# Performance work log

Hardware: AMD Instinct MI355X
Metric: run time of the kernel (lower is better)

The kernel has to match this reference:

```python
import jax, jax.numpy as jnp
import numpy as np

B, N, D = 8, 2048, 1024
H, HD, FF = 16, 32, 4096  # head_dim = D // H // 2 = 32
LAMBDA_INIT = float(0.8 - 0.6 * np.exp(-0.3 * 1.0))  # layer_num = 1
EPS = 1e-5


def setup_inputs() -> dict:
    key = jax.random.key(0)
    ks = jax.random.split(key, 24)
    g = lambda k, shape, std=0.02: (jax.random.normal(k, shape, jnp.float32) * std)
    return {
        "src": jax.random.normal(ks[0], (B, N, D), jnp.float32),
        "Wq": g(ks[1], (D, D)), "Wk": g(ks[2], (D, D)), "Wv": g(ks[3], (D, D)),
        "Wo": g(ks[4], (D, D)), "bo": jnp.zeros((D,), jnp.float32),
        "lq1": g(ks[5], (HD,), 0.1), "lq2": g(ks[6], (HD,), 0.1),
        "lk1": g(ks[7], (HD,), 0.1), "lk2": g(ks[8], (HD,), 0.1),
        "ln1_g": jnp.ones((D,), jnp.float32), "ln1_b": jnp.zeros((D,), jnp.float32),
        "ln2_g": jnp.ones((D,), jnp.float32), "ln2_b": jnp.zeros((D,), jnp.float32),
        "W1": g(ks[9], (FF, D)), "b1": jnp.zeros((FF,), jnp.float32),
        "W2": g(ks[10], (D, FF)), "b2": jnp.zeros((D,), jnp.float32),
        "Wr": g(ks[11], (D, D)), "Ur": g(ks[12], (D, D)),
        "Wz": g(ks[13], (D, D)), "Uz": g(ks[14], (D, D)),
        "Wg": g(ks[15], (D, D)), "Ug": g(ks[16], (D, D)),
        "bg": jnp.full((D,), 2.0, jnp.float32),
    }


def _layernorm(x, gamma, beta):
    m = x.mean(-1, keepdims=True)
    v = jnp.mean((x - m) ** 2, axis=-1, keepdims=True)
    return (x - m) * jax.lax.rsqrt(v + EPS) * gamma + beta


def _diff_attn(x, Wq, Wk, Wv, Wo, bo, lq1, lq2, lk1, lk2):
    b, n, d = x.shape
    scale = HD ** -0.5
    # 'b n (h d q) -> b n (q h) d'
    q = (x @ Wq.T).reshape(b, n, H, HD, 2).transpose(0, 1, 4, 2, 3).reshape(b, n, 2 * H, HD) * scale
    # 'b n (h d k) -> b n (k h) d'
    k = (x @ Wk.T).reshape(b, n, H, HD, 2).transpose(0, 1, 4, 2, 3).reshape(b, n, 2 * H, HD)
    # 'b n (h d) -> b h n d', d = 2*HD
    v = (x @ Wv.T).reshape(b, n, H, 2 * HD).transpose(0, 2, 1, 3)
    # per-token attention over the 2H head axis: [b, n, 2H, 2H]
    att = jnp.einsum('bnqd,bnkd->bnqk', q, k)
    att = jax.nn.softmax(att.astype(jnp.float32), axis=-1)
    lam = jnp.exp(jnp.sum(lq1 * lk1)) - jnp.exp(jnp.sum(lq2 * lk2)) + LAMBDA_INIT
    att = att.reshape(b, n, 2, H, 2, H)  # q k split
    diff = att[:, :, 0, :, 0, :] - lam * att[:, :, 1, :, 1, :]  # [b, n, H, H]
    out = jnp.einsum('bnah,bhnd->bnad', diff, v)  # [b, n, H, 2*HD]
    # RMSNorm over last dim, no affine
    out = out * jax.lax.rsqrt(jnp.mean(out ** 2, axis=-1, keepdims=True) + EPS)
    out = (out * (1.0 - LAMBDA_INIT)).reshape(b, n, d)
    return out @ Wo.T + bo


def _gate_gru(x, y, Wr, Ur, Wz, Uz, Wg, Ug, bg):
    r = jax.nn.sigmoid(y @ Wr.T + x @ Ur.T)
    z = jax.nn.sigmoid(y @ Wz.T + x @ Uz.T - bg)
    h = jnp.tanh(y @ Wg.T + (r * x) @ Ug.T)
    return (1.0 - z) * x + z * h


def reference(src, Wq, Wk, Wv, Wo, bo, lq1, lq2, lk1, lk2,
              ln1_g, ln1_b, ln2_g, ln2_b, W1, b1, W2, b2,
              Wr, Ur, Wz, Uz, Wg, Ug, bg):
    # norm_first=True, use_gate=True (GRU), wo_ffn=False, dropout=0 (eval)
    s = _layernorm(src, ln1_g, ln1_b)
    src2 = _diff_attn(s, Wq, Wk, Wv, Wo, bo, lq1, lq2, lk1, lk2)
    conn = _gate_gru(src, jax.nn.relu(src2), Wr, Ur, Wz, Uz, Wg, Ug, bg)
    c = _layernorm(conn, ln2_g, ln2_b)
    src3 = jax.nn.relu(c @ W1.T + b1) @ W2.T + b2
    conn2 = _gate_gru(conn, jax.nn.relu(src3), Wr, Ur, Wz, Uz, Wg, Ug, bg)
    return conn2
```

## Files before the change

kernel.cpp:

```cpp
#include <hip/hip_runtime.h>


#define DEV __device__ __forceinline__

typedef unsigned short u16;
typedef __bf16 bf16x8 __attribute__((ext_vector_type(8)));
typedef float f32x4 __attribute__((ext_vector_type(4)));
typedef unsigned short us8 __attribute__((ext_vector_type(8)));
typedef unsigned short us4 __attribute__((ext_vector_type(4)));

#define LAMBDA0            0.35550906759096928f
#define ONE_MINUS_LAMBDA0  0.6444909324090307f
#define QSCALE             0.17677669529663687f

DEV float bf2f(u16 u) { union { unsigned u; float f; } x; x.u = ((unsigned)u) << 16; return x.f; }
DEV u16 f2bf(float f) {
  union { float f; unsigned u; } x; x.f = f;
  unsigned r = x.u + 0x7FFFu + ((x.u >> 16) & 1u);
  return (u16)(r >> 16);
}

DEV void gl_lds16(const void* g, void* l) {
  __builtin_amdgcn_global_load_lds((__attribute__((address_space(1))) void*)g,
                                   (__attribute__((address_space(3))) void*)l, 16, 0, 0);
}

#define MF(a, b, c) __builtin_amdgcn_mfma_f32_16x16x32_bf16(a, b, c, 0, 0, 0)
#define BARM() asm volatile("s_barrier" ::: "memory")

DEV void stage_half_f(const u16* __restrict__ g, int ld, int rowbase, int k0,
                      u16* lds, int bufoff , int h, int wave, int lane)
{
  const int rr = lane >> 3;
  const int sc = ((lane & 7) ^ rr) * 8;
  const u16* gs = g + (size_t)(rowbase + h * 128 + wave * 16 + rr) * ld + (k0 + sc);
  u16* l = lds + bufoff + h * 8192 + wave * 1024;
  gl_lds16(gs, l);
  gl_lds16(gs + (size_t)8 * ld, l + 512);
}

template <int ACT, int OBF>
__global__ __launch_bounds__(512, 2)
void gemm256(const u16* __restrict__ A, int lda, const u16* __restrict__ W,
             const float* __restrict__ bias, void* __restrict__ outp,
             int ldo, int K)
{
  __shared__ u16 As[32768];
  __shared__ u16 Bs[32768];

  const int tid = threadIdx.x;
  const int lane = tid & 63, wave = tid >> 6;
  const int wr = wave >> 2, wc = wave & 3;
  const int frow = lane & 15, fx = lane >> 4, s7 = lane & 7;

  const int gx = gridDim.x;
  const int nwg = gx * gridDim.y;
  const int lin = blockIdx.y * gx + blockIdx.x;
  const int logical = (lin & 7) * (nwg >> 3) + (lin >> 3);
  const int m0 = (logical / gx) * 256;
  const int n0 = (logical % gx) * 256;

  const int NT = K >> 6;
  const int aoff = (wr * 32 + frow) * 64;
  const int boff = (wc * 64 + frow) * 64;
  const int swA0 = (fx ^ s7) * 8;
  const int swA1 = ((4 + fx) ^ s7) * 8;

  f32x4 acc[8][4] = {};
  bf16x8 bfr[4][2];

  stage_half_f(W, K, n0, 0, Bs, 0, 0, wave, lane);
  stage_half_f(W, K, n0, 0, Bs, 0, 1, wave, lane);
  stage_half_f(A, lda, m0, 0, As, 0, 0, wave, lane);
  stage_half_f(A, lda, m0, 0, As, 0, 1, wave, lane);
  stage_half_f(W, K, n0, 64, Bs, 16384, 0, wave, lane);
  stage_half_f(W, K, n0, 64, Bs, 16384, 1, wave, lane);
  asm volatile("s_waitcnt vmcnt(6)" ::: "memory");
  BARM();

#define PH(q, STG, TAILW)                                                     \
  {                                                                           \
    bf16x8 a00 = *(const bf16x8*)(As + aB + 4096 * (q) + swA0);               \
    bf16x8 a01 = *(const bf16x8*)(As + aB + 4096 * (q) + swA1);               \
    bf16x8 a10 = *(const bf16x8*)(As + aB + 4096 * (q) + 1024 + swA0);        \
    bf16x8 a11 = *(const bf16x8*)(As + aB + 4096 * (q) + 1024 + swA1);        \
    STG;                                                                      \
    BARM();                                                                   \
    __builtin_amdgcn_s_setprio(1);                                            \
    acc[2*(q)  ][0] = MF(a00, bfr[0][0], acc[2*(q)  ][0]);                    \
    acc[2*(q)  ][1] = MF(a00, bfr[1][0], acc[2*(q)  ][1]);                    \
    acc[2*(q)  ][2] = MF(a00, bfr[2][0], acc[2*(q)  ][2]);                    \
    acc[2*(q)  ][3] = MF(a00, bfr[3][0], acc[2*(q)  ][3]);                    \
    acc[2*(q)+1][0] = MF(a10, bfr[0][0], acc[2*(q)+1][0]);                    \
    acc[2*(q)+1][1] = MF(a10, bfr[1][0], acc[2*(q)+1][1]);                    \
    acc[2*(q)+1][2] = MF(a10, bfr[2][0], acc[2*(q)+1][2]);                    \
    acc[2*(q)+1][3] = MF(a10, bfr[3][0], acc[2*(q)+1][3]);                    \
    acc[2*(q)  ][0] = MF(a01, bfr[0][1], acc[2*(q)  ][0]);                    \
    acc[2*(q)  ][1] = MF(a01, bfr[1][1], acc[2*(q)  ][1]);                    \
    acc[2*(q)  ][2] = MF(a01, bfr[2][1], acc[2*(q)  ][2]);                    \
    acc[2*(q)  ][3] = MF(a01, bfr[3][1], acc[2*(q)  ][3]);                    \
    acc[2*(q)+1][0] = MF(a11, bfr[0][1], acc[2*(q)+1][0]);                    \
    acc[2*(q)+1][1] = MF(a11, bfr[1][1], acc[2*(q)+1][1]);                    \
    acc[2*(q)+1][2] = MF(a11, bfr[2][1], acc[2*(q)+1][2]);                    \
    acc[2*(q)+1][3] = MF(a11, bfr[3][1], acc[2*(q)+1][3]);                    \
    __builtin_amdgcn_s_setprio(0);                                            \
    TAILW;                                                                    \
    BARM();                                                                   \
  }

  for (int t = 0; t < NT; ++t) {
    const int cb = (t & 1) * 16384;
    const int ob = 16384 - cb;
    const int kA = ((t + 1 < NT) ? t + 1 : NT - 1) * 64;
    const int kB = ((t + 2 < NT) ? t + 2 : NT - 1) * 64;
    const int aB = cb + aoff;
    const int bB = cb + boff;
#pragma unroll
    for (int n = 0; n < 4; ++n) {
      bfr[n][0] = *(const bf16x8*)(Bs + bB + n * 1024 + swA0);
      bfr[n][1] = *(const bf16x8*)(Bs + bB + n * 1024 + swA1);
    }
    PH(0, stage_half_f(A, lda, m0, kA, As, ob, 0, wave, lane), (void)0);
    PH(1, stage_half_f(A, lda, m0, kA, As, ob, 1, wave, lane),
       asm volatile("s_waitcnt vmcnt(8)" ::: "memory"));
    PH(2, stage_half_f(W, K, n0, kB, Bs, cb, 0, wave, lane), (void)0);
    PH(3, stage_half_f(W, K, n0, kB, Bs, cb, 1, wave, lane),
       asm volatile("s_waitcnt vmcnt(6)" ::: "memory"));
  }
#undef PH

  const int er = fx * 4;
#pragma unroll
  for (int q = 0; q < 4; ++q)
#pragma unroll
    for (int j = 0; j < 2; ++j) {
      const int grb = m0 + 64 * q + wr * 32 + j * 16 + er;
#pragma unroll
      for (int n = 0; n < 4; ++n) {
        const int gc = n0 + wc * 64 + n * 16 + frow;
        const float bv = bias ? bias[gc] : 0.f;
#pragma unroll
        for (int tt = 0; tt < 4; ++tt) {
          float v = acc[2 * q + j][n][tt] + bv;
          if (ACT == 1) v = fmaxf(v, 0.f);
          else if (ACT == 2) v = 1.f / (1.f + expf(-v));
          else if (ACT == 3) v = tanhf(v);
          if (OBF) ((u16*)outp)[(size_t)(grb + tt) * ldo + gc] = f2bf(v);
          else     ((float*)outp)[(size_t)(grb + tt) * ldo + gc] = v;
        }
      }
    }
}

__global__ __launch_bounds__(256)
void ln_kernel(const float* __restrict__ in, const float* __restrict__ g,
               const float* __restrict__ b, u16* __restrict__ out)
{
  const int row = blockIdx.x, tid = threadIdx.x;
  const float4 x = ((const float4*)(in + (size_t)row * 1024))[tid];
  float s = x.x + x.y + x.z + x.w;
  float sq = x.x * x.x + x.y * x.y + x.z * x.z + x.w * x.w;
#pragma unroll
  for (int o = 32; o >= 1; o >>= 1) { s += __shfl_xor(s, o); sq += __shfl_xor(sq, o); }
  __shared__ float ls[4], lq[4];
  const int wave = tid >> 6;
  if ((tid & 63) == 0) { ls[wave] = s; lq[wave] = sq; }
  __syncthreads();
  s = ls[0] + ls[1] + ls[2] + ls[3];
  sq = lq[0] + lq[1] + lq[2] + lq[3];
  const float mean = s * (1.f / 1024.f);
  const float rstd = rsqrtf(sq * (1.f / 1024.f) - mean * mean + 1e-5f);
  const float4 gg = ((const float4*)g)[tid];
  const float4 bb = ((const float4*)b)[tid];
  us4 ov;
  ov[0] = f2bf((x.x - mean) * rstd * gg.x + bb.x);
  ov[1] = f2bf((x.y - mean) * rstd * gg.y + bb.y);
  ov[2] = f2bf((x.z - mean) * rstd * gg.z + bb.z);
  ov[3] = f2bf((x.w - mean) * rstd * gg.w + bb.w);
  *(us4*)(out + (size_t)row * 1024 + tid * 4) = ov;
}

__global__ __launch_bounds__(256)
void combine_ln_kernel(const float* __restrict__ x, const float* __restrict__ rzh,
                       const float* __restrict__ g, const float* __restrict__ b,
                       float* __restrict__ conn, u16* __restrict__ catbase)
{
  const int row = blockIdx.x, tid = threadIdx.x;
  const float4 xv = ((const float4*)(x + (size_t)row * 1024))[tid];
  const float4 hv = *(const float4*)(rzh + (size_t)row * 2048 + tid * 4);
  const float4 zv = *(const float4*)(rzh + (size_t)row * 2048 + 1024 + tid * 4);
  float4 cv;
  cv.x = (1.f - zv.x) * xv.x + zv.x * hv.x;
  cv.y = (1.f - zv.y) * xv.y + zv.y * hv.y;
  cv.z = (1.f - zv.z) * xv.z + zv.z * hv.z;
  cv.w = (1.f - zv.w) * xv.w + zv.w * hv.w;
  ((float4*)(conn + (size_t)row * 1024))[tid] = cv;
  us4 cb; cb[0] = f2bf(cv.x); cb[1] = f2bf(cv.y); cb[2] = f2bf(cv.z); cb[3] = f2bf(cv.w);
  *(us4*)(catbase + (size_t)row * 2048 + 1024 + tid * 4) = cb;

  float s = cv.x + cv.y + cv.z + cv.w;
  float sq = cv.x * cv.x + cv.y * cv.y + cv.z * cv.z + cv.w * cv.w;
#pragma unroll
  for (int o = 32; o >= 1; o >>= 1) { s += __shfl_xor(s, o); sq += __shfl_xor(sq, o); }
  __shared__ float ls[4], lq[4];
  const int wave = tid >> 6;
  if ((tid & 63) == 0) { ls[wave] = s; lq[wave] = sq; }
  __syncthreads();
  s = ls[0] + ls[1] + ls[2] + ls[3];
  sq = lq[0] + lq[1] + lq[2] + lq[3];
  const float mean = s * (1.f / 1024.f);
  const float rstd = rsqrtf(sq * (1.f / 1024.f) - mean * mean + 1e-5f);
  const float4 gg = ((const float4*)g)[tid];
  const float4 bb = ((const float4*)b)[tid];
  us4 ov;
  ov[0] = f2bf((cv.x - mean) * rstd * gg.x + bb.x);
  ov[1] = f2bf((cv.y - mean) * rstd * gg.y + bb.y);
  ov[2] = f2bf((cv.z - mean) * rstd * gg.z + bb.z);
  ov[3] = f2bf((cv.w - mean) * rstd * gg.w + bb.w);
  *(us4*)(catbase + (size_t)row * 2048 + tid * 4) = ov;
}

__global__ __launch_bounds__(256)
void combine2_kernel(const float* __restrict__ x, const float* __restrict__ rzh,
                     float* __restrict__ out)
{
  const int t = blockIdx.x * 256 + threadIdx.x;
  const int row = t >> 8;
  const int c4 = (t & 255) * 4;
  const float4 hv = *(const float4*)(rzh + (size_t)row * 2048 + c4);
  const float4 zv = *(const float4*)(rzh + (size_t)row * 2048 + 1024 + c4);
  const float4 xv = *(const float4*)(x + (size_t)row * 1024 + c4);
  float4 o;
  o.x = (1.f - zv.x) * xv.x + zv.x * hv.x;
  o.y = (1.f - zv.y) * xv.y + zv.y * hv.y;
  o.z = (1.f - zv.z) * xv.z + zv.z * hv.z;
  o.w = (1.f - zv.w) * xv.w + zv.w * hv.w;
  *(float4*)(out + (size_t)row * 1024 + c4) = o;
}

__global__ __launch_bounds__(256)
void rx_kernel(const float* __restrict__ rzh, const float* __restrict__ x,
               u16* __restrict__ dst)
{
  const int t = blockIdx.x * 256 + threadIdx.x;
  const int row = t >> 8;
  const int c4 = (t & 255) * 4;
  const float4 rv = *(const float4*)(rzh + (size_t)row * 2048 + c4);
  const float4 xv = *(const float4*)(x + (size_t)row * 1024 + c4);
  us4 o;
  o[0] = f2bf(rv.x * xv.x); o[1] = f2bf(rv.y * xv.y);
  o[2] = f2bf(rv.z * xv.z); o[3] = f2bf(rv.w * xv.w);
  *(us4*)(dst + (size_t)row * 2048 + c4) = o;
}

__global__ __launch_bounds__(256)
void cvt2d_kernel(const float* __restrict__ src, u16* __restrict__ dst,
                  int total4, int cshift, int ldd)
{
  const int t = blockIdx.x * 256 + threadIdx.x;
  if (t >= total4) return;
  const int idx = t * 4;
  const int r = idx >> cshift;
  const int c = idx & ((1 << cshift) - 1);
  const float4 v = *(const float4*)(src + (size_t)idx);
  us4 o; o[0] = f2bf(v.x); o[1] = f2bf(v.y); o[2] = f2bf(v.z); o[3] = f2bf(v.w);
  *(us4*)(dst + (size_t)r * ldd + c) = o;
}

__global__ __launch_bounds__(256)
void biasrz_kernel(const float* __restrict__ bg, float* __restrict__ brz)
{
  const int t = blockIdx.x * 256 + threadIdx.x;
  brz[t] = (t < 1024) ? 0.f : -bg[t - 1024];
}

__global__ __launch_bounds__(256)
void sentinel_kernel(float* __restrict__ out, int n)
{
  const int t = blockIdx.x * 256 + threadIdx.x;
  if (t < n) out[t] = 1.0e9f;
}

__global__ __launch_bounds__(256)
void attn_kernel(const u16* __restrict__ qkv,
                 const float* __restrict__ lq1, const float* __restrict__ lq2,
                 const float* __restrict__ lk1, const float* __restrict__ lk2,
                 u16* __restrict__ out)
{
  __shared__ float k_s[4][32][36];
  __shared__ float att_s[4][32][33];
  const int wave = threadIdx.x >> 6, lane = threadIdx.x & 63;
  const int tok = blockIdx.x * 4 + wave;
  const u16* qrow = qkv + (size_t)tok * 3072;
  const u16* krow = qrow + 1024;
  const u16* vrow = qrow + 2048;

  {
    us8 a = *(const us8*)(krow + lane * 16);
    us8 b = *(const us8*)(krow + lane * 16 + 8);
#pragma unroll
    for (int j = 0; j < 16; ++j) {
      int e = lane * 16 + j;
      u16 usv = (j < 8) ? a[j] : b[j - 8];
      int h = e >> 6, r = e & 63;
      k_s[wave][(r & 1) * 16 + h][r >> 1] = bf2f(usv);
    }
  }
  float qr[32];
  {
    const int a = lane & 31, h = a & 15, qi = a >> 4;
#pragma unroll
    for (int s = 0; s < 8; ++s) {
      us8 v8 = *(const us8*)(qrow + h * 64 + s * 8);
#pragma unroll
      for (int u = 0; u < 4; ++u) qr[s * 4 + u] = bf2f(v8[2 * u + qi]) * QSCALE;
    }
  }
  float lam;
  {
    const int dd = lane & 31;
    float p1 = lq1[dd] * lk1[dd], p2 = lq2[dd] * lk2[dd];
#pragma unroll
    for (int o = 16; o >= 1; o >>= 1) { p1 += __shfl_xor(p1, o); p2 += __shfl_xor(p2, o); }
    lam = expf(p1) - expf(p2) + LAMBDA0;
  }
  __syncthreads();

  const int a = lane & 31, bb = (lane >> 5) * 16;
  float av[16];
#pragma unroll
  for (int bi = 0; bi < 16; ++bi) {
    const float4* kk = (const float4*)&k_s[wave][bb + bi][0];
    float s = 0.f;
#pragma unroll
    for (int d4 = 0; d4 < 8; ++d4) {
      float4 kv = kk[d4];
      s += qr[d4 * 4 + 0] * kv.x + qr[d4 * 4 + 1] * kv.y +
           qr[d4 * 4 + 2] * kv.z + qr[d4 * 4 + 3] * kv.w;
    }
    av[bi] = s;
  }
  float mx = av[0];
#pragma unroll
  for (int i = 1; i < 16; ++i) mx = fmaxf(mx, av[i]);
  mx = fmaxf(mx, __shfl_xor(mx, 32));
  float se = 0.f;
#pragma unroll
  for (int i = 0; i < 16; ++i) { av[i] = expf(av[i] - mx); se += av[i]; }
  se += __shfl_xor(se, 32);
  const float inv = 1.f / se;
#pragma unroll
  for (int i = 0; i < 16; ++i) att_s[wave][a][bb + i] = av[i] * inv;
  __syncthreads();

  const int a2 = lane >> 2, jb = (lane & 3) * 16;
  float o[16];
#pragma unroll
  for (int j = 0; j < 16; ++j) o[j] = 0.f;
#pragma unroll
  for (int h = 0; h < 16; ++h) {
    const float dc = att_s[wave][a2][h] - lam * att_s[wave][16 + a2][16 + h];
    const u16* vv = vrow + h * 64 + jb;
    us8 v0 = *(const us8*)vv;
    us8 v1 = *(const us8*)(vv + 8);
#pragma unroll
    for (int j = 0; j < 8; ++j) { o[j] += dc * bf2f(v0[j]); o[8 + j] += dc * bf2f(v1[j]); }
  }
  float ss = 0.f;
#pragma unroll
  for (int j = 0; j < 16; ++j) ss += o[j] * o[j];
  ss += __shfl_xor(ss, 1);
  ss += __shfl_xor(ss, 2);
  const float sc = rsqrtf(ss * (1.f / 64.f) + 1e-5f) * ONE_MINUS_LAMBDA0;
  us8 r0, r1;
#pragma unroll
  for (int j = 0; j < 8; ++j) { r0[j] = f2bf(o[j] * sc); r1[j] = f2bf(o[8 + j] * sc); }
  u16* op = out + (size_t)tok * 1024 + a2 * 64 + jb;
  *(us8*)op = r0;
  *(us8*)(op + 8) = r1;
}

enum : size_t {
  OFF_WQKV = 0,
  OFF_WO   = OFF_WQKV + (size_t)3072 * 1024 * 2,
  OFF_WRZ  = OFF_WO   + (size_t)1024 * 1024 * 2,
  OFF_WG   = OFF_WRZ  + (size_t)2048 * 2048 * 2,
  OFF_W1   = OFF_WG   + (size_t)1024 * 2048 * 2,
  OFF_W2   = OFF_W1   + (size_t)4096 * 1024 * 2,
  OFF_BRZ  = OFF_W2   + (size_t)1024 * 4096 * 2,
  OFF_R1   = OFF_BRZ  + (size_t)2048 * 4,
  OFF_CAT  = OFF_R1   + (size_t)134217728,
  WS_NEED  = OFF_CAT  + (size_t)16384 * 2048 * 2
};

extern "C" void kernel_launch(void* const* d_in, const int* in_sizes, int n_in,
                              void* d_out, int out_size, void* d_ws, size_t ws_size,
                              hipStream_t stream)
{
  (void)in_sizes; (void)n_in;
  if (ws_size < WS_NEED) {
    sentinel_kernel<<<(out_size + 255) / 256, 256, 0, stream>>>((float*)d_out, out_size);
    return;
  }

  const float* src  = (const float*)d_in[0];
  const float* Wq   = (const float*)d_in[1];
  const float* Wk   = (const float*)d_in[2];
  const float* Wv   = (const float*)d_in[3];
  const float* Wo   = (const float*)d_in[4];
  const float* bo   = (const float*)d_in[5];
  const float* lq1  = (const float*)d_in[6];
  const float* lq2  = (const float*)d_in[7];
  const float* lk1  = (const float*)d_in[8];
  const float* lk2  = (const float*)d_in[9];
  const float* ln1g = (const float*)d_in[10];
  const float* ln1b = (const float*)d_in[11];
  const float* ln2g = (const float*)d_in[12];
  const float* ln2b = (const float*)d_in[13];
  const float* W1   = (const float*)d_in[14];
  const float* b1   = (const float*)d_in[15];
  const float* W2   = (const float*)d_in[16];
  const float* b2   = (const float*)d_in[17];
  const float* Wr   = (const float*)d_in[18];
  const float* Ur   = (const float*)d_in[19];
  const float* Wz   = (const float*)d_in[20];
  const float* Uz   = (const float*)d_in[21];
  const float* Wg   = (const float*)d_in[22];
  const float* Ug   = (const float*)d_in[23];
  const float* bg   = (const float*)d_in[24];

  char* ws = (char*)d_ws;
  u16*   wqkv = (u16*)(ws + OFF_WQKV);
  u16*   wo_b = (u16*)(ws + OFF_WO);
  u16*   wrz  = (u16*)(ws + OFF_WRZ);
  u16*   wgc  = (u16*)(ws + OFF_WG);
  u16*   w1b  = (u16*)(ws + OFF_W1);
  u16*   w2b  = (u16*)(ws + OFF_W2);
  float* brz  = (float*)(ws + OFF_BRZ);
  u16*   r1u  = (u16*)(ws + OFF_R1);
  u16*   sbuf = (u16*)(ws + OFF_R1 + 100663296);
  float* rzh  = (float*)(ws + OFF_R1);
  u16*   cat  = (u16*)(ws + OFF_CAT);
  float* conn = (float*)d_out;

  auto cvt = [&](const float* s, u16* dst, int rows, int cshift, int ldd) {
    int total4 = (rows << cshift) >> 2;
    cvt2d_kernel<<<(total4 + 255) / 256, 256, 0, stream>>>(s, dst, total4, cshift, ldd);
  };

  cvt(Wq, wqkv,                     1024, 10, 1024);
  cvt(Wk, wqkv + 1024 * 1024,       1024, 10, 1024);
  cvt(Wv, wqkv + 2 * 1024 * 1024,   1024, 10, 1024);
  cvt(Wo, wo_b,                     1024, 10, 1024);
  cvt(Wr, wrz,                      1024, 10, 2048);
  cvt(Ur, wrz + 1024,               1024, 10, 2048);
  cvt(Wz, wrz + 2048 * 1024,        1024, 10, 2048);
  cvt(Uz, wrz + 2048 * 1024 + 1024, 1024, 10, 2048);
  cvt(Wg, wgc,                      1024, 10, 2048);
  cvt(Ug, wgc + 1024,               1024, 10, 2048);
  cvt(W1, w1b,                      4096, 10, 1024);
  cvt(W2, w2b,                      1024, 12, 4096);
  cvt(src, cat + 1024,             16384, 10, 2048);
  biasrz_kernel<<<8, 256, 0, stream>>>(bg, brz);

  ln_kernel<<<16384, 256, 0, stream>>>(src, ln1g, ln1b, sbuf);

  gemm256<0, 1><<<dim3(12, 64), 512, 0, stream>>>(sbuf, 1024, wqkv, nullptr, r1u, 3072, 1024);

  attn_kernel<<<4096, 256, 0, stream>>>(r1u, lq1, lq2, lk1, lk2, sbuf);

  gemm256<1, 1><<<dim3(4, 64), 512, 0, stream>>>(sbuf, 1024, wo_b, bo, cat, 2048, 1024);

  gemm256<2, 0><<<dim3(8, 64), 512, 0, stream>>>(cat, 2048, wrz, brz, rzh, 2048, 2048);
  rx_kernel<<<16384, 256, 0, stream>>>(rzh, src, cat + 1024);
  gemm256<3, 0><<<dim3(4, 64), 512, 0, stream>>>(cat, 2048, wgc, nullptr, rzh, 2048, 2048);
  combine_ln_kernel<<<16384, 256, 0, stream>>>(src, rzh, ln2g, ln2b, conn, cat);

  gemm256<1, 1><<<dim3(16, 64), 512, 0, stream>>>(cat, 2048, w1b, b1, r1u, 4096, 1024);
  gemm256<1, 1><<<dim3(4, 64), 512, 0, stream>>>(r1u, 4096, w2b, b2, cat, 2048, 4096);

  gemm256<2, 0><<<dim3(8, 64), 512, 0, stream>>>(cat, 2048, wrz, brz, rzh, 2048, 2048);
  rx_kernel<<<16384, 256, 0, stream>>>(rzh, conn, cat + 1024);
  gemm256<3, 0><<<dim3(4, 64), 512, 0, stream>>>(cat, 2048, wgc, nullptr, rzh, 2048, 2048);
  combine2_kernel<<<16384, 256, 0, stream>>>(conn, rzh, (float*)d_out);
}
```

Before: 1.318 ms.

## Switch GEMM to 32x32x16 MFMA tiles with reworked LDS pipeline

Replaces the 16x16x32 bf16 MFMA inner loop with 32x32x16 MFMA, reorganising per-wave fragments into 4x2 32x32 accumulators and loading B fragments once per K tile. The staging schedule is restructured into two phases per K step, with A prefetch issued up front and W prefetch in the second phase and adjusted vmcnt waits. The epilogue is rewritten for the 32x32 output layout. Larger MFMA tiles reduce LDS fragment reads per FLOP, at the risk of a changed pipeline overlap and more register pressure.

```diff
diff --git a/kernel.cpp b/kernel.cpp
--- a/kernel.cpp
+++ b/kernel.cpp
@@ -6,6 +6,7 @@
 typedef unsigned short u16;
 typedef __bf16 bf16x8 __attribute__((ext_vector_type(8)));
 typedef float f32x4 __attribute__((ext_vector_type(4)));
+typedef float f32x16 __attribute__((ext_vector_type(16)));
 typedef unsigned short us8 __attribute__((ext_vector_type(8)));
 typedef unsigned short us4 __attribute__((ext_vector_type(4)));
 
@@ -25,7 +26,7 @@
                                    (__attribute__((address_space(3))) void*)l, 16, 0, 0);
 }
 
-#define MF(a, b, c) __builtin_amdgcn_mfma_f32_16x16x32_bf16(a, b, c, 0, 0, 0)
+#define MF32(a, b, c) __builtin_amdgcn_mfma_f32_32x32x16_bf16(a, b, c, 0, 0, 0)
 #define BARM() asm volatile("s_barrier" ::: "memory")
 
 DEV void stage_half_f(const u16* __restrict__ g, int ld, int rowbase, int k0,
@@ -51,7 +52,7 @@
   const int tid = threadIdx.x;
   const int lane = tid & 63, wave = tid >> 6;
   const int wr = wave >> 2, wc = wave & 3;
-  const int frow = lane & 15, fx = lane >> 4, s7 = lane & 7;
+  const int r31 = lane & 31, fx32 = lane >> 5, l7 = lane & 7;
 
   const int gx = gridDim.x;
   const int nwg = gx * gridDim.y;
@@ -61,48 +62,53 @@
   const int n0 = (logical % gx) * 256;
 
   const int NT = K >> 6;
-  const int aoff = (wr * 32 + frow) * 64;
-  const int boff = (wc * 64 + frow) * 64;
-  const int swA0 = (fx ^ s7) * 8;
-  const int swA1 = ((4 + fx) ^ s7) * 8;
-
-  f32x4 acc[8][4] = {};
-  bf16x8 bfr[4][2];
-
+  const int sw[4] = { ((0 + fx32) ^ l7) * 8, ((2 + fx32) ^ l7) * 8,
+                      ((4 + fx32) ^ l7) * 8, ((6 + fx32) ^ l7) * 8 };
+  const int arow = (wr * 32 + r31) * 64;
+  const int brow = (wc * 64 + r31) * 64;
+
+  f32x16 acc[4][2] = {};
+  bf16x8 bb[2][4];
+
+  stage_half_f(A, lda, m0, 0, As, 0, 0, wave, lane);
+  stage_half_f(A, lda, m0, 0, As, 0, 1, wave, lane);
   stage_half_f(W, K, n0, 0, Bs, 0, 0, wave, lane);
   stage_half_f(W, K, n0, 0, Bs, 0, 1, wave, lane);
-  stage_half_f(A, lda, m0, 0, As, 0, 0, wave, lane);
-  stage_half_f(A, lda, m0, 0, As, 0, 1, wave, lane);
   stage_half_f(W, K, n0, 64, Bs, 16384, 0, wave, lane);
   stage_half_f(W, K, n0, 64, Bs, 16384, 1, wave, lane);
-  asm volatile("s_waitcnt vmcnt(6)" ::: "memory");
+  asm volatile("s_waitcnt vmcnt(4)" ::: "memory");
   BARM();
 
-#define PH(q, STG, TAILW)                                                     \
+#define PH32(p, STG, TAILW)                                                   \
   {                                                                           \
-    bf16x8 a00 = *(const bf16x8*)(As + aB + 4096 * (q) + swA0);               \
-    bf16x8 a01 = *(const bf16x8*)(As + aB + 4096 * (q) + swA1);               \
-    bf16x8 a10 = *(const bf16x8*)(As + aB + 4096 * (q) + 1024 + swA0);        \
-    bf16x8 a11 = *(const bf16x8*)(As + aB + 4096 * (q) + 1024 + swA1);        \
     STG;                                                                      \
+    const int mb = cb + (p) * 8192 + arow;                                    \
+    bf16x8 a00 = *(const bf16x8*)(As + mb + sw[0]);                           \
+    bf16x8 a01 = *(const bf16x8*)(As + mb + sw[1]);                           \
+    bf16x8 a02 = *(const bf16x8*)(As + mb + sw[2]);                           \
+    bf16x8 a03 = *(const bf16x8*)(As + mb + sw[3]);                           \
+    bf16x8 a10 = *(const bf16x8*)(As + mb + 4096 + sw[0]);                    \
+    bf16x8 a11 = *(const bf16x8*)(As + mb + 4096 + sw[1]);                    \
+    bf16x8 a12 = *(const bf16x8*)(As + mb + 4096 + sw[2]);                    \
+    bf16x8 a13 = *(const bf16x8*)(As + mb + 4096 + sw[3]);                    \
     BARM();                                                                   \
     __builtin_amdgcn_s_setprio(1);                                            \
-    acc[2*(q)  ][0] = MF(a00, bfr[0][0], acc[2*(q)  ][0]);                    \
-    acc[2*(q)  ][1] = MF(a00, bfr[1][0], acc[2*(q)  ][1]);                    \
-    acc[2*(q)  ][2] = MF(a00, bfr[2][0], acc[2*(q)  ][2]);                    \
-    acc[2*(q)  ][3] = MF(a00, bfr[3][0], acc[2*(q)  ][3]);                    \
-    acc[2*(q)+1][0] = MF(a10, bfr[0][0], acc[2*(q)+1][0]);                    \
-    acc[2*(q)+1][1] = MF(a10, bfr[1][0], acc[2*(q)+1][1]);                    \
-    acc[2*(q)+1][2] = MF(a10, bfr[2][0], acc[2*(q)+1][2]);                    \
-    acc[2*(q)+1][3] = MF(a10, bfr[3][0], acc[2*(q)+1][3]);                    \
-    acc[2*(q)  ][0] = MF(a01, bfr[0][1], acc[2*(q)  ][0]);                    \
-    acc[2*(q)  ][1] = MF(a01, bfr[1][1], acc[2*(q)  ][1]);                    \
-    acc[2*(q)  ][2] = MF(a01, bfr[2][1], acc[2*(q)  ][2]);                    \
-    acc[2*(q)  ][3] = MF(a01, bfr[3][1], acc[2*(q)  ][3]);                    \
-    acc[2*(q)+1][0] = MF(a11, bfr[0][1], acc[2*(q)+1][0]);                    \
-    acc[2*(q)+1][1] = MF(a11, bfr[1][1], acc[2*(q)+1][1]);                    \
-    acc[2*(q)+1][2] = MF(a11, bfr[2][1], acc[2*(q)+1][2]);                    \
-    acc[2*(q)+1][3] = MF(a11, bfr[3][1], acc[2*(q)+1][3]);                    \
+    acc[2*(p)  ][0] = MF32(a00, bb[0][0], acc[2*(p)  ][0]);                   \
+    acc[2*(p)  ][1] = MF32(a00, bb[1][0], acc[2*(p)  ][1]);                   \
+    acc[2*(p)+1][0] = MF32(a10, bb[0][0], acc[2*(p)+1][0]);                   \
+    acc[2*(p)+1][1] = MF32(a10, bb[1][0], acc[2*(p)+1][1]);                   \
+    acc[2*(p)  ][0] = MF32(a01, bb[0][1], acc[2*(p)  ][0]);                   \
+    acc[2*(p)  ][1] = MF32(a01, bb[1][1], acc[2*(p)  ][1]);                   \
+    acc[2*(p)+1][0] = MF32(a11, bb[0][1], acc[2*(p)+1][0]);                   \
+    acc[2*(p)+1][1] = MF32(a11, bb[1][1], acc[2*(p)+1][1]);                   \
+    acc[2*(p)  ][0] = MF32(a02, bb[0][2], acc[2*(p)  ][0]);                   \
+    acc[2*(p)  ][1] = MF32(a02, bb[1][2], acc[2*(p)  ][1]);                   \
+    acc[2*(p)+1][0] = MF32(a12, bb[0][2], acc[2*(p)+1][0]);                   \
+    acc[2*(p)+1][1] = MF32(a12, bb[1][2], acc[2*(p)+1][1]);                   \
+    acc[2*(p)  ][0] = MF32(a03, bb[0][3], acc[2*(p)  ][0]);                   \
+    acc[2*(p)  ][1] = MF32(a03, bb[1][3], acc[2*(p)  ][1]);                   \
+    acc[2*(p)+1][0] = MF32(a13, bb[0][3], acc[2*(p)+1][0]);                   \
+    acc[2*(p)+1][1] = MF32(a13, bb[1][3], acc[2*(p)+1][1]);                   \
     __builtin_amdgcn_s_setprio(0);                                            \
     TAILW;                                                                    \
     BARM();                                                                   \
@@ -113,41 +119,38 @@
     const int ob = 16384 - cb;
     const int kA = ((t + 1 < NT) ? t + 1 : NT - 1) * 64;
     const int kB = ((t + 2 < NT) ? t + 2 : NT - 1) * 64;
-    const int aB = cb + aoff;
-    const int bB = cb + boff;
-#pragma unroll
-    for (int n = 0; n < 4; ++n) {
-      bfr[n][0] = *(const bf16x8*)(Bs + bB + n * 1024 + swA0);
-      bfr[n][1] = *(const bf16x8*)(Bs + bB + n * 1024 + swA1);
+    {
+      stage_half_f(A, lda, m0, kA, As, ob, 0, wave, lane);
+      stage_half_f(A, lda, m0, kA, As, ob, 1, wave, lane);
+#pragma unroll
+      for (int nj = 0; nj < 2; ++nj)
+#pragma unroll
+        for (int ks = 0; ks < 4; ++ks)
+          bb[nj][ks] = *(const bf16x8*)(Bs + cb + brow + nj * 2048 + sw[ks]);
     }
-    PH(0, stage_half_f(A, lda, m0, kA, As, ob, 0, wave, lane), (void)0);
-    PH(1, stage_half_f(A, lda, m0, kA, As, ob, 1, wave, lane),
-       asm volatile("s_waitcnt vmcnt(8)" ::: "memory"));
-    PH(2, stage_half_f(W, K, n0, kB, Bs, cb, 0, wave, lane), (void)0);
-    PH(3, stage_half_f(W, K, n0, kB, Bs, cb, 1, wave, lane),
-       asm volatile("s_waitcnt vmcnt(6)" ::: "memory"));
-  }
-#undef PH
-
-  const int er = fx * 4;
-#pragma unroll
-  for (int q = 0; q < 4; ++q)
-#pragma unroll
-    for (int j = 0; j < 2; ++j) {
-      const int grb = m0 + 64 * q + wr * 32 + j * 16 + er;
-#pragma unroll
-      for (int n = 0; n < 4; ++n) {
-        const int gc = n0 + wc * 64 + n * 16 + frow;
-        const float bv = bias ? bias[gc] : 0.f;
-#pragma unroll
-        for (int tt = 0; tt < 4; ++tt) {
-          float v = acc[2 * q + j][n][tt] + bv;
-          if (ACT == 1) v = fmaxf(v, 0.f);
-          else if (ACT == 2) v = 1.f / (1.f + expf(-v));
-          else if (ACT == 3) v = tanhf(v);
-          if (OBF) ((u16*)outp)[(size_t)(grb + tt) * ldo + gc] = f2bf(v);
-          else     ((float*)outp)[(size_t)(grb + tt) * ldo + gc] = v;
-        }
+    PH32(0, (void)0, (void)0);
+    PH32(1,
+         { stage_half_f(W, K, n0, kB, Bs, cb, 0, wave, lane);
+           stage_half_f(W, K, n0, kB, Bs, cb, 1, wave, lane); },
+         asm volatile("s_waitcnt vmcnt(4)" ::: "memory"));
+  }
+#undef PH32
+
+#pragma unroll
+  for (int mi = 0; mi < 4; ++mi)
+#pragma unroll
+    for (int nj = 0; nj < 2; ++nj) {
+      const int gc = n0 + wc * 64 + nj * 32 + r31;
+      const float bv = bias ? bias[gc] : 0.f;
+#pragma unroll
+      for (int tt = 0; tt < 16; ++tt) {
+        const int gr = m0 + mi * 64 + wr * 32 + (tt & 3) + 8 * (tt >> 2) + 4 * fx32;
+        float v = acc[mi][nj][tt] + bv;
+        if (ACT == 1) v = fmaxf(v, 0.f);
+        else if (ACT == 2) v = 1.f / (1.f + expf(-v));
+        else if (ACT == 3) v = tanhf(v);
+        if (OBF) ((u16*)outp)[(size_t)gr * ldo + gc] = f2bf(v);
+        else     ((float*)outp)[(size_t)gr * ldo + gc] = v;
       }
     }
 }
```

After: 1.331 ms. Within noise of the previous version (+1.0%).

## Fuse GRU gate elementwise ops into GEMM epilogues and split-source A loads

Applied to the files above, without the earlier changes.

The sigmoid-r times x product and the z output move into the r/z GEMM epilogue, and the tanh plus GRU blend moves into the gate GEMM epilogue. This removes the separate rx, combine and combine2 kernels. The gate GEMM now reads its A operand from two buffers, split at column 1024, so r*x can live in its own buffer instead of being written back into the concat buffer. LayerNorm 2 becomes a plain ln_kernel over conn. The aim is to cut several full-size fp32 round trips through HBM and some launches. In exchange, the epilogues do scattered scalar loads of x and z, and the final GEMM reads and writes conn in place.

```diff
diff --git a/kernel.cpp b/kernel.cpp
--- a/kernel.cpp
+++ b/kernel.cpp
@@ -39,19 +39,32 @@
   gl_lds16(gs + (size_t)8 * ld, l + 512);
 }
 
-template <int ACT, int OBF>
+template <int ACT, int MODE>
 __global__ __launch_bounds__(512, 2)
-void gemm256(const u16* __restrict__ A, int lda, const u16* __restrict__ W,
+void gemm256(const u16* __restrict__ A, int lda,
+             const u16* __restrict__ A2, int lda2, int ksplit,
+             const u16* __restrict__ W,
              const float* __restrict__ bias, void* __restrict__ outp,
-             int ldo, int K)
+             int ldo, int K,
+             const float* __restrict__ xp, const float* __restrict__ zb,
+             u16* __restrict__ bfd)
 {
   __shared__ u16 As[32768];
   __shared__ u16 Bs[32768];
 
   const int tid = threadIdx.x;
   const int lane = tid & 63, wave = tid >> 6;
-  const int wr = wave >> 2, wc = wave & 3;
-  const int frow = lane & 15, fx = lane >> 4, s7 = lane & 7;
+  const int wr = wave >> 1, wc = wave & 1;
+  const int wm = (wave >> 1) * 0;
+  (void)wr; (void)wc; (void)wm;
+  const int wmr = (wave >> 2) * 0;
+  (void)wmr;
+
+  const int wMh = (wave >> 2);
+  const int wN  = (wave & 3);
+  const int frow = lane & 15;
+  const int fk = lane >> 4;
+  const int s7 = lane & 7;
 
   const int gx = gridDim.x;
   const int nwg = gx * gridDim.y;
@@ -61,18 +74,24 @@
   const int n0 = (logical % gx) * 256;
 
   const int NT = K >> 6;
-  const int aoff = (wr * 32 + frow) * 64;
-  const int boff = (wc * 64 + frow) * 64;
-  const int swA0 = (fx ^ s7) * 8;
-  const int swA1 = ((4 + fx) ^ s7) * 8;
+  const int aoff = (wMh * 32 + frow) * 64;
+  const int boff = (wN * 64 + frow) * 64;
+  const int swA0 = (fk ^ s7) * 8;
+  const int swA1 = ((4 + fk) ^ s7) * 8;
 
   f32x4 acc[8][4] = {};
   bf16x8 bfr[4][2];
 
+  auto stageA = [&](int kcol, int bufoff, int h) {
+    const u16* base = A; int ld = lda; int kc = kcol;
+    if (A2 && kcol >= ksplit) { base = A2; ld = lda2; kc = kcol - ksplit; }
+    stage_half_f(base, ld, m0, kc, As, bufoff, h, wave, lane);
+  };
+
   stage_half_f(W, K, n0, 0, Bs, 0, 0, wave, lane);
   stage_half_f(W, K, n0, 0, Bs, 0, 1, wave, lane);
-  stage_half_f(A, lda, m0, 0, As, 0, 0, wave, lane);
-  stage_half_f(A, lda, m0, 0, As, 0, 1, wave, lane);
+  stageA(0, 0, 0);
+  stageA(0, 0, 1);
   stage_half_f(W, K, n0, 64, Bs, 16384, 0, wave, lane);
   stage_half_f(W, K, n0, 64, Bs, 16384, 1, wave, lane);
   asm volatile("s_waitcnt vmcnt(6)" ::: "memory");
@@ -120,8 +139,8 @@
       bfr[n][0] = *(const bf16x8*)(Bs + bB + n * 1024 + swA0);
       bfr[n][1] = *(const bf16x8*)(Bs + bB + n * 1024 + swA1);
     }
-    PH(0, stage_half_f(A, lda, m0, kA, As, ob, 0, wave, lane), (void)0);
-    PH(1, stage_half_f(A, lda, m0, kA, As, ob, 1, wave, lane),
+    PH(0, stageA(kA, ob, 0), (void)0);
+    PH(1, stageA(kA, ob, 1),
        asm volatile("s_waitcnt vmcnt(8)" ::: "memory"));
     PH(2, stage_half_f(W, K, n0, kB, Bs, cb, 0, wave, lane), (void)0);
     PH(3, stage_half_f(W, K, n0, kB, Bs, cb, 1, wave, lane),
@@ -129,32 +148,48 @@
   }
 #undef PH
 
-  const int er = fx * 4;
-#pragma unroll
-  for (int q = 0; q < 4; ++q)
-#pragma unroll
-    for (int j = 0; j < 2; ++j) {
-      const int grb = m0 + 64 * q + wr * 32 + j * 16 + er;
-#pragma unroll
-      for (int n = 0; n < 4; ++n) {
-        const int gc = n0 + wc * 64 + n * 16 + frow;
-        const float bv = bias ? bias[gc] : 0.f;
+  const int ec = lane & 15;
+  const int er = (lane >> 4) * 4;
+#pragma unroll
+  for (int j = 0; j < 4; ++j) {
+    const int gc = n0 + wN * 64 + j * 16 + ec;
+    const float bv = bias ? bias[gc] : 0.f;
+#pragma unroll
+    for (int q = 0; q < 4; ++q)
+#pragma unroll
+      for (int i = 0; i < 2; ++i) {
+        const int grb = m0 + 64 * q + wMh * 32 + i * 16 + er;
 #pragma unroll
         for (int tt = 0; tt < 4; ++tt) {
-          float v = acc[2 * q + j][n][tt] + bv;
+          const int row = grb + tt;
+          float v = acc[2 * q + i][j][tt] + bv;
           if (ACT == 1) v = fmaxf(v, 0.f);
-          else if (ACT == 2) v = 1.f / (1.f + expf(-v));
-          else if (ACT == 3) v = tanhf(v);
-          if (OBF) ((u16*)outp)[(size_t)(grb + tt) * ldo + gc] = f2bf(v);
-          else     ((float*)outp)[(size_t)(grb + tt) * ldo + gc] = v;
+          if (MODE == 0) {
+            ((u16*)outp)[(size_t)row * ldo + gc] = f2bf(v);
+          } else if (MODE == 1) {
+            ((float*)outp)[(size_t)row * ldo + gc] = v;
+          } else if (MODE == 2) {
+            const float rv = 1.f / (1.f + expf(-v));
+            if (gc < 1024)
+              bfd[(size_t)row * 1024 + gc] = f2bf(rv * xp[(size_t)row * 1024 + gc]);
+            else
+              ((float*)outp)[(size_t)row * 1024 + (gc - 1024)] = rv;
+          } else {
+            const float hv = tanhf(v);
+            const float z = zb[(size_t)row * 1024 + gc];
+            const float x = xp[(size_t)row * 1024 + gc];
+            const float c = (1.f - z) * x + z * hv;
+            ((float*)outp)[(size_t)row * 1024 + gc] = c;
+            if (MODE == 3) bfd[(size_t)row * 2048 + gc] = f2bf(c);
+          }
         }
       }
-    }
+  }
 }
 
 __global__ __launch_bounds__(256)
 void ln_kernel(const float* __restrict__ in, const float* __restrict__ g,
-               const float* __restrict__ b, u16* __restrict__ out)
+               const float* __restrict__ b, u16* __restrict__ out, int ldo)
 {
   const int row = blockIdx.x, tid = threadIdx.x;
   const float4 x = ((const float4*)(in + (size_t)row * 1024))[tid];
@@ -177,80 +212,7 @@
   ov[1] = f2bf((x.y - mean) * rstd * gg.y + bb.y);
   ov[2] = f2bf((x.z - mean) * rstd * gg.z + bb.z);
   ov[3] = f2bf((x.w - mean) * rstd * gg.w + bb.w);
-  *(us4*)(out + (size_t)row * 1024 + tid * 4) = ov;
-}
-
-__global__ __launch_bounds__(256)
-void combine_ln_kernel(const float* __restrict__ x, const float* __restrict__ rzh,
-                       const float* __restrict__ g, const float* __restrict__ b,
-                       float* __restrict__ conn, u16* __restrict__ catbase)
-{
-  const int row = blockIdx.x, tid = threadIdx.x;
-  const float4 xv = ((const float4*)(x + (size_t)row * 1024))[tid];
-  const float4 hv = *(const float4*)(rzh + (size_t)row * 2048 + tid * 4);
-  const float4 zv = *(const float4*)(rzh + (size_t)row * 2048 + 1024 + tid * 4);
-  float4 cv;
-  cv.x = (1.f - zv.x) * xv.x + zv.x * hv.x;
-  cv.y = (1.f - zv.y) * xv.y + zv.y * hv.y;
-  cv.z = (1.f - zv.z) * xv.z + zv.z * hv.z;
-  cv.w = (1.f - zv.w) * xv.w + zv.w * hv.w;
-  ((float4*)(conn + (size_t)row * 1024))[tid] = cv;
-  us4 cb; cb[0] = f2bf(cv.x); cb[1] = f2bf(cv.y); cb[2] = f2bf(cv.z); cb[3] = f2bf(cv.w);
-  *(us4*)(catbase + (size_t)row * 2048 + 1024 + tid * 4) = cb;
-
-  float s = cv.x + cv.y + cv.z + cv.w;
-  float sq = cv.x * cv.x + cv.y * cv.y + cv.z * cv.z + cv.w * cv.w;
-#pragma unroll
-  for (int o = 32; o >= 1; o >>= 1) { s += __shfl_xor(s, o); sq += __shfl_xor(sq, o); }
-  __shared__ float ls[4], lq[4];
-  const int wave = tid >> 6;
-  if ((tid & 63) == 0) { ls[wave] = s; lq[wave] = sq; }
-  __syncthreads();
-  s = ls[0] + ls[1] + ls[2] + ls[3];
-  sq = lq[0] + lq[1] + lq[2] + lq[3];
-  const float mean = s * (1.f / 1024.f);
-  const float rstd = rsqrtf(sq * (1.f / 1024.f) - mean * mean + 1e-5f);
-  const float4 gg = ((const float4*)g)[tid];
-  const float4 bb = ((const float4*)b)[tid];
-  us4 ov;
-  ov[0] = f2bf((cv.x - mean) * rstd * gg.x + bb.x);
-  ov[1] = f2bf((cv.y - mean) * rstd * gg.y + bb.y);
-  ov[2] = f2bf((cv.z - mean) * rstd * gg.z + bb.z);
-  ov[3] = f2bf((cv.w - mean) * rstd * gg.w + bb.w);
-  *(us4*)(catbase + (size_t)row * 2048 + tid * 4) = ov;
-}
-
-__global__ __launch_bounds__(256)
-void combine2_kernel(const float* __restrict__ x, const float* __restrict__ rzh,
-                     float* __restrict__ out)
-{
-  const int t = blockIdx.x * 256 + threadIdx.x;
-  const int row = t >> 8;
-  const int c4 = (t & 255) * 4;
-  const float4 hv = *(const float4*)(rzh + (size_t)row * 2048 + c4);
-  const float4 zv = *(const float4*)(rzh + (size_t)row * 2048 + 1024 + c4);
-  const float4 xv = *(const float4*)(x + (size_t)row * 1024 + c4);
-  float4 o;
-  o.x = (1.f - zv.x) * xv.x + zv.x * hv.x;
-  o.y = (1.f - zv.y) * xv.y + zv.y * hv.y;
-  o.z = (1.f - zv.z) * xv.z + zv.z * hv.z;
-  o.w = (1.f - zv.w) * xv.w + zv.w * hv.w;
-  *(float4*)(out + (size_t)row * 1024 + c4) = o;
-}
-
-__global__ __launch_bounds__(256)
-void rx_kernel(const float* __restrict__ rzh, const float* __restrict__ x,
-               u16* __restrict__ dst)
-{
-  const int t = blockIdx.x * 256 + threadIdx.x;
-  const int row = t >> 8;
-  const int c4 = (t & 255) * 4;
-  const float4 rv = *(const float4*)(rzh + (size_t)row * 2048 + c4);
-  const float4 xv = *(const float4*)(x + (size_t)row * 1024 + c4);
-  us4 o;
-  o[0] = f2bf(rv.x * xv.x); o[1] = f2bf(rv.y * xv.y);
-  o[2] = f2bf(rv.z * xv.z); o[3] = f2bf(rv.w * xv.w);
-  *(us4*)(dst + (size_t)row * 2048 + c4) = o;
+  *(us4*)(out + (size_t)row * ldo + tid * 4) = ov;
 }
 
 __global__ __launch_bounds__(256)
@@ -438,8 +400,9 @@
   u16*   w2b  = (u16*)(ws + OFF_W2);
   float* brz  = (float*)(ws + OFF_BRZ);
   u16*   r1u  = (u16*)(ws + OFF_R1);
+  float* zbuf = (float*)(ws + OFF_R1);
+  u16*   rxbuf= (u16*)(ws + OFF_R1 + 67108864);
   u16*   sbuf = (u16*)(ws + OFF_R1 + 100663296);
-  float* rzh  = (float*)(ws + OFF_R1);
   u16*   cat  = (u16*)(ws + OFF_CAT);
   float* conn = (float*)d_out;
 
@@ -463,24 +426,37 @@
   cvt(src, cat + 1024,             16384, 10, 2048);
   biasrz_kernel<<<8, 256, 0, stream>>>(bg, brz);
 
-  ln_kernel<<<16384, 256, 0, stream>>>(src, ln1g, ln1b, sbuf);
-
-  gemm256<0, 1><<<dim3(12, 64), 512, 0, stream>>>(sbuf, 1024, wqkv, nullptr, r1u, 3072, 1024);
+  ln_kernel<<<16384, 256, 0, stream>>>(src, ln1g, ln1b, sbuf, 1024);
+
+  gemm256<0, 0><<<dim3(12, 64), 512, 0, stream>>>(
+      sbuf, 1024, nullptr, 0, 1024, wqkv, nullptr, r1u, 3072, 1024,
+      nullptr, nullptr, nullptr);
 
   attn_kernel<<<4096, 256, 0, stream>>>(r1u, lq1, lq2, lk1, lk2, sbuf);
 
-  gemm256<1, 1><<<dim3(4, 64), 512, 0, stream>>>(sbuf, 1024, wo_b, bo, cat, 2048, 1024);
-
-  gemm256<2, 0><<<dim3(8, 64), 512, 0, stream>>>(cat, 2048, wrz, brz, rzh, 2048, 2048);
-  rx_kernel<<<16384, 256, 0, stream>>>(rzh, src, cat + 1024);
-  gemm256<3, 0><<<dim3(4, 64), 512, 0, stream>>>(cat, 2048, wgc, nullptr, rzh, 2048, 2048);
-  combine_ln_kernel<<<16384, 256, 0, stream>>>(src, rzh, ln2g, ln2b, conn, cat);
-
-  gemm256<1, 1><<<dim3(16, 64), 512, 0, stream>>>(cat, 2048, w1b, b1, r1u, 4096, 1024);
-  gemm256<1, 1><<<dim3(4, 64), 512, 0, stream>>>(r1u, 4096, w2b, b2, cat, 2048, 4096);
-
-  gemm256<2, 0><<<dim3(8, 64), 512, 0, stream>>>(cat, 2048, wrz, brz, rzh, 2048, 2048);
-  rx_kernel<<<16384, 256, 0, stream>>>(rzh, conn, cat + 1024);
-  gemm256<3, 0><<<dim3(4, 64), 512, 0, stream>>>(cat, 2048, wgc, nullptr, rzh, 2048, 2048);
-  combine2_kernel<<<16384, 256, 0, stream>>>(conn, rzh, (float*)d_out);
-}
+  gemm256<1, 0><<<dim3(4, 64), 512, 0, stream>>>(
+      sbuf, 1024, nullptr, 0, 1024, wo_b, bo, cat, 2048, 1024,
+      nullptr, nullptr, nullptr);
+
+  gemm256<0, 2><<<dim3(8, 64), 512, 0, stream>>>(
+      cat, 2048, nullptr, 0, 2048, wrz, brz, zbuf, 1024, 2048,
+      src, nullptr, rxbuf);
+  gemm256<0, 3><<<dim3(4, 64), 512, 0, stream>>>(
+      cat, 2048, rxbuf, 1024, 1024, wgc, nullptr, conn, 1024, 2048,
+      src, zbuf, cat + 1024);
+  ln_kernel<<<16384, 256, 0, stream>>>(conn, ln2g, ln2b, cat, 2048);
+
+  gemm256<1, 0><<<dim3(16, 64), 512, 0, stream>>>(
+      cat, 2048, nullptr, 0, 1024, w1b, b1, r1u, 4096, 1024,
+      nullptr, nullptr, nullptr);
+  gemm256<1, 0><<<dim3(4, 64), 512, 0, stream>>>(
+      r1u, 4096, nullptr, 0, 4096, w2b, b2, cat, 2048, 4096,
+      nullptr, nullptr, nullptr);
+
+  gemm256<0, 2><<<dim3(8, 64), 512, 0, stream>>>(
+      cat, 2048, nullptr, 0, 2048, wrz, brz, zbuf, 1024, 2048,
+      conn, nullptr, rxbuf);
+  gemm256<0, 4><<<dim3(4, 64), 512, 0, stream>>>(
+      cat, 2048, rxbuf, 1024, 1024, wgc, nullptr, (float*)d_out, 1024, 2048,
+      conn, zbuf, nullptr);
+}
```

Result: slower. 1.715 ms (+30.1%).
